# Kernel tuning notes

Measured on AMD Instinct MI355X. Metric: run time of the kernel, lower is better.

## Reference

```python
import jax, jax.numpy as jnp
import numpy as np

B, S, L = 256, 2048, 64  # batch, seq_len, label_size (= num_labels + 2)
START, END = L - 2, L - 1


def setup_inputs() -> dict:
    key = jax.random.key(0)
    k1, k2, k3, k4 = jax.random.split(key, 4)
    logits = jax.random.normal(k1, (B, S, L), dtype=jnp.float32)
    # pad_logits: <SOS>/<EOS> score columns are -100
    logits = logits.at[:, :, START:].set(-100.0)
    transition = jax.random.normal(k2, (L, L), dtype=jnp.float32)
    # CRF.initialize(): nothing transitions into end-as-source / out of start-as-target
    transition = transition.at[:, END].set(-100.0)
    transition = transition.at[START, :].set(-100.0)
    labels = jax.random.randint(k3, (B, S), 0, L - 2, dtype=jnp.int32)
    lens = jnp.maximum(jax.random.randint(k4, (B,), 1, S + 1, dtype=jnp.int32), 1)
    return {"logits": logits, "transition": transition, "labels": labels, "lens": lens}


def _loglik(logits, transition, labels, lens):
    Bc, Sc, Lc = logits.shape
    dt = logits.dtype
    mask_s = (jnp.arange(Sc)[None, :] < lens[:, None])  # [B,S] valid-token mask

    # ---- gold unary score: sum_t logits[b, t, labels[b,t]] over valid t ----
    unary = jnp.take_along_axis(logits, labels[..., None].astype(jnp.int32), axis=2)[..., 0]
    gold_unary = jnp.sum(unary * mask_s.astype(dt), axis=1)  # [B]

    # ---- gold binary score: transition[to, from] along extended label path ----
    lab_ext = jnp.concatenate(
        [jnp.full((Bc, 1), START, labels.dtype), labels, jnp.full((Bc, 1), END, labels.dtype)],
        axis=1,
    )  # [B, S+2]
    m_ext = jnp.arange(Sc + 2)[None, :] < (lens + 1)[:, None]
    lab_ext = jnp.where(m_ext, lab_ext, END)  # positions past lens become <EOS>
    trn_scr = transition[lab_ext[:, 1:], lab_ext[:, :-1]]  # [B, S+1]
    m_trn = (jnp.arange(Sc + 1)[None, :] < (lens + 1)[:, None]).astype(dt)
    gold_binary = jnp.sum(trn_scr * m_trn, axis=1)  # [B]
    gold = gold_unary + gold_binary

    # ---- norm score: forward algorithm (log-semiring scan over time) ----
    alpha0 = jnp.full((Bc, Lc), -100.0, dtype=dt).at[:, START].set(0.0)

    def step(alpha, inp):
        logit, active = inp  # logit: [B,L], active: [B]
        # mat[b, to, frm] = logit[b,to] + alpha[b,frm] + transition[to,frm]
        mat = logit[:, :, None] + alpha[:, None, :] + transition[None, :, :]
        alpha_nxt = jax.nn.logsumexp(mat, axis=2)  # [B,L]
        alpha = jnp.where(active[:, None], alpha_nxt, alpha)
        return alpha, None

    alpha, _ = jax.lax.scan(step, alpha0, (jnp.swapaxes(logits, 0, 1), mask_s.T))
    norm = jax.nn.logsumexp(alpha + transition[END][None, :], axis=1)  # [B]

    return gold - norm


def reference(logits, transition, labels, lens):
    return _loglik(logits, transition, labels, lens)
```

## Files before the change

kernel.cpp:

```cpp
#include <hip/hip_runtime.h>


#define Bsz 256
#define Ssz 2048
#define START_ 62
#define END_ 63
#define PSTRIDE 36

typedef __attribute__((ext_vector_type(2))) _Float16 half2v;
typedef __attribute__((ext_vector_type(8))) _Float16 half8;
typedef __attribute__((ext_vector_type(16))) float f32x16;

__device__ __forceinline__ unsigned pack_pkrtz(float a, float b) {
    auto h = __builtin_amdgcn_cvt_pkrtz(a, b);
    return __builtin_bit_cast(unsigned, h);
}

__device__ __forceinline__ float dot2h(unsigned a, unsigned b, float c) {
#if __has_builtin(__builtin_amdgcn_fdot2)
    return __builtin_amdgcn_fdot2(__builtin_bit_cast(half2v, a),
                                  __builtin_bit_cast(half2v, b), c, false);
#else
    half2v ha = __builtin_bit_cast(half2v, a);
    half2v hb = __builtin_bit_cast(half2v, b);
    c = __builtin_fmaf((float)ha.x, (float)hb.x, c);
    return __builtin_fmaf((float)ha.y, (float)hb.y, c);
#endif
}

__device__ __forceinline__ float wave_sum(float v) {
#pragma unroll
    for (int m = 32; m >= 1; m >>= 1) v += __shfl_xor(v, m, 64);
    return v;
}

#define CRF_STEP(LG)                                                           \
    {                                                                          \
        const float l_ = __builtin_amdgcn_exp2f((LG) * L2E);                   \
        const int nbi_ = __builtin_amdgcn_update_dpp(                          \
            0, __float_as_int(E), 0xB1, 0xf, 0xf, true);                       \
        const unsigned packed_ = pack_pkrtz(E, __int_as_float(nbi_));          \
        float c0 = 0.f, c1 = 0.f, c2 = 0.f, c3 = 0.f;                          \
        float c4 = 0.f, c5 = 0.f, c6 = 0.f, c7 = 0.f;                          \
        _Pragma("unroll")                                                      \
        for (int k8 = 0; k8 < 8; ++k8) {                                       \
            const uint4 q_ = q[k8];                                            \
            const unsigned t0 = (unsigned)__builtin_amdgcn_readlane(           \
                (int)packed_, 8 * k8 + 0);                                     \
            const unsigned t1 = (unsigned)__builtin_amdgcn_readlane(           \
                (int)packed_, 8 * k8 + 2);                                     \
            const unsigned t2 = (unsigned)__builtin_amdgcn_readlane(           \
                (int)packed_, 8 * k8 + 4);                                     \
            const unsigned t3 = (unsigned)__builtin_amdgcn_readlane(           \
                (int)packed_, 8 * k8 + 6);                                     \
            if (k8 & 1) {                                                      \
                c4 = dot2h(t0, q_.x, c4);                                      \
                c5 = dot2h(t1, q_.y, c5);                                      \
                c6 = dot2h(t2, q_.z, c6);                                      \
                c7 = dot2h(t3, q_.w, c7);                                      \
            } else {                                                           \
                c0 = dot2h(t0, q_.x, c0);                                      \
                c1 = dot2h(t1, q_.y, c1);                                      \
                c2 = dot2h(t2, q_.z, c2);                                      \
                c3 = dot2h(t3, q_.w, c3);                                      \
            }                                                                  \
        }                                                                      \
        const float y_ = ((c0 + c1) + (c2 + c3)) + ((c4 + c5) + (c6 + c7));    \
        const float Ey_ = y_ * l_;                                             \
        const int pb_ = __builtin_amdgcn_readlane(__float_as_int(Ey_), 0);     \
        const int ee_ = (pb_ >> 23) & 0xff;                                    \
        const float sc_ = __int_as_float((244 - ee_) << 23);                   \
        E = Ey_ * sc_;                                                         \
        D += ee_ - 117;                                                        \
    }

#define LOAD_QBLOCK()                                                          \
    {                                                                          \
        unsigned off_ = (unsigned)(lane * (PSTRIDE * 4));                      \
        asm volatile("" : "+v"(off_));                                         \
        const uint4* prow_ = (const uint4*)((const char*)Psh + off_);          \
        _Pragma("unroll")                                                      \
        for (int k8 = 0; k8 < 8; ++k8) q[k8] = prow_[k8];                      \
    }

__global__ __launch_bounds__(64)
__attribute__((amdgpu_waves_per_eu(1, 1)))
void crf_kernel(const float* __restrict__ logits,
                const float* __restrict__ transition,
                const int* __restrict__ labels,
                const int* __restrict__ lens,
                float* __restrict__ out)
{
    const int b    = blockIdx.x;
    const int lane = threadIdx.x;
    const float L2E = 1.4426950408889634f;
    const float LN2 = 0.6931471805599453f;

    __shared__ unsigned Psh[64 * PSTRIDE];

    const int len = lens[b];
    const float* lrow = logits + (size_t)b * (Ssz * 64);

#pragma unroll
    for (int k = 0; k < 32; ++k) {
        float p0 = __builtin_amdgcn_exp2f(transition[lane * 64 + 2 * k]     * L2E);
        float p1 = __builtin_amdgcn_exp2f(transition[lane * 64 + 2 * k + 1] * L2E);
        Psh[lane * PSTRIDE + k] = pack_pkrtz(p0, p1);
    }
    asm volatile("s_waitcnt lgkmcnt(0)" ::: "memory");

    float E = (lane == START_) ? 1.0f : 0.0f;
    int   D = 0;

    float lgb[8];
#pragma unroll
    for (int d = 0; d < 8; ++d) {
        int s0 = (d < len) ? d : (len - 1);
        lgb[d] = lrow[s0 * 64 + lane];
    }

    uint4 q[8];
    const int len8 = len & ~7;
    for (int s = 0; s < len8; s += 8) {
        LOAD_QBLOCK();
#pragma unroll
        for (int d = 0; d < 8; ++d) {
            const float lg = lgb[d];
            int pf = s + 8 + d;
            pf = (pf < len) ? pf : (len - 1);
            lgb[d] = lrow[pf * 64 + lane];
            CRF_STEP(lg);
        }
    }
    const int rem = len - len8;
    if (rem) {
        LOAD_QBLOCK();
        for (int d = 0; d < rem; ++d) {
            const float lg = lgb[d];
            CRF_STEP(lg);
        }
    }

    const float Pend = __builtin_amdgcn_exp2f(transition[END_ * 64 + lane] * L2E);
    const float tot  = wave_sum(E * Pend);
    const float norm = LN2 * ((float)D + __builtin_amdgcn_logf(tot));

    const int* lab = labels + (size_t)b * Ssz;
    float g = 0.0f;
    for (int s = lane; s < len; s += 64) {
        const int l1 = lab[s];
        const int l0 = (s == 0) ? START_ : lab[s - 1];
        g += lrow[s * 64 + l1] + transition[l1 * 64 + l0];
    }
    if (lane == 0) g += transition[END_ * 64 + lab[len - 1]];
    const float gold = wave_sum(g);

    if (lane == 0) out[b] = gold - norm;
}


#define MF16(Aop, Bop, Cop) \
    __builtin_amdgcn_mfma_f32_32x32x16_f16((Aop), (Bop), (Cop), 0, 0, 0)

#define STEP_COMPUTE(LGA, LGB)                                                 \
    f32x16 a00, a10;                                                           \
    {                                                                          \
        const float ncf_ = -(float)ci;                                         \
        const float lv0_ = __builtin_amdgcn_exp2f(                             \
            __builtin_fmaf((LGA), L2E, ncf_));                                 \
        const float lv1_ = __builtin_amdgcn_exp2f(                             \
            __builtin_fmaf((LGB), L2E, ncf_));                                 \
        D += ci;                                                               \
        const _Float16 h0_ = (_Float16)lv0_;                                   \
        const _Float16 h1_ = (_Float16)lv1_;                                   \
        const half8 sv0_ = {h0_, h0_, h0_, h0_, h0_, h0_, h0_, h0_};           \
        const half8 sv1_ = {h1_, h1_, h1_, h1_, h1_, h1_, h1_, h1_};           \
        half8 A_;                                                              \
        __builtin_amdgcn_s_setprio(1);                                         \
        A_ = __builtin_bit_cast(half8, PF[0][0]) * sv0_;                       \
        a00 = MF16(A_, __builtin_bit_cast(half8, Bf[0]), Z);                   \
        A_ = __builtin_bit_cast(half8, PF[0][1]) * sv0_;                       \
        a00 = MF16(A_, __builtin_bit_cast(half8, Bf[1]), a00);                 \
        A_ = __builtin_bit_cast(half8, PF[0][2]) * sv0_;                       \
        a00 = MF16(A_, __builtin_bit_cast(half8, Bf[2]), a00);                 \
        A_ = __builtin_bit_cast(half8, PF[0][3]) * sv0_;                       \
        a00 = MF16(A_, __builtin_bit_cast(half8, Bf[3]), a00);                 \
        A_ = __builtin_bit_cast(half8, PF[1][0]) * sv1_;                       \
        a10 = MF16(A_, __builtin_bit_cast(half8, Bf[0]), Z);                   \
        A_ = __builtin_bit_cast(half8, PF[1][1]) * sv1_;                       \
        a10 = MF16(A_, __builtin_bit_cast(half8, Bf[1]), a10);                 \
        A_ = __builtin_bit_cast(half8, PF[1][2]) * sv1_;                       \
        a10 = MF16(A_, __builtin_bit_cast(half8, Bf[2]), a10);                 \
        A_ = __builtin_bit_cast(half8, PF[1][3]) * sv1_;                       \
        a10 = MF16(A_, __builtin_bit_cast(half8, Bf[3]), a10);                 \
        __builtin_amdgcn_s_setprio(0);                                         \
        const float t0_ = fmaxf(fmaxf(a00[0], a00[1]), a00[2]);                \
        const float t1_ = fmaxf(fmaxf(a00[3], a00[4]), a00[5]);                \
        const float t2_ = fmaxf(fmaxf(a00[6], a00[7]), a00[8]);                \
        const float t3_ = fmaxf(fmaxf(a00[9], a00[10]), a00[11]);              \
        const float t4_ = fmaxf(fmaxf(a00[12], a00[13]), a00[14]);             \
        const float ma_ = fmaxf(fmaxf(t0_, t1_), t2_);                         \
        const float mb2_ = fmaxf(fmaxf(t3_, t4_), a00[15]);                    \
        const int mb_ = __builtin_amdgcn_readfirstlane(                        \
            __float_as_int(fmaxf(ma_, mb2_)));                                 \
        int cin_ = ((mb_ >> 23) & 0xff) - 121;      \
        cin_ = (cin_ < -60) ? -60 : cin_;                                      \
        ci = (cin_ > 60) ? 60 : cin_;                                          \
    }

#define TILE_TO_FRAGS(ACC, BD0, BD1)                                           \
    {                                                                          \
        (BD0) = make_uint4(pack_pkrtz(ACC[0], ACC[1]),                         \
                           pack_pkrtz(ACC[2], ACC[3]),                         \
                           pack_pkrtz(ACC[4], ACC[5]),                         \
                           pack_pkrtz(ACC[6], ACC[7]));                        \
        (BD1) = make_uint4(pack_pkrtz(ACC[8], ACC[9]),                         \
                           pack_pkrtz(ACC[10], ACC[11]),                       \
                           pack_pkrtz(ACC[12], ACC[13]),                       \
                           pack_pkrtz(ACC[14], ACC[15]));                      \
    }

#define STEP_FULL(LGA, LGB)                                                    \
    {                                                                          \
        STEP_COMPUTE(LGA, LGB);                                                \
        TILE_TO_FRAGS(a00, Bf[0], Bf[1]);                                      \
        TILE_TO_FRAGS(a10, Bf[2], Bf[3]);                                      \
    }

#define STEP_LAST(LGA, LGB)                                                    \
    {                                                                          \
        STEP_COMPUTE(LGA, LGB);                                                \
        float* gout_ = Gws + (size_t)gslot * 4096 + nb * 32;                   \
        _Pragma("unroll")                                                      \
        for (int r = 0; r < 16; ++r) {                                         \
            const int row0_ = (r & 3) + 8 * (r >> 2) + 4 * hi;                 \
            gout_[row0_ * 64 + lo5]        = a00[r];                           \
            gout_[(row0_ + 32) * 64 + lo5] = a10[r];                           \
        }                                                                      \
        if (lo5 == 0 && hi == 0) Dws[gslot * 2 + nb] = D;                      \
    }

template<int CHT>
__global__ __launch_bounds__(128)
__attribute__((amdgpu_waves_per_eu(4, 8)))
void crf_chunk(const float* __restrict__ logits,
               const float* __restrict__ transition,
               const int* __restrict__ lens,
               float* __restrict__ Gws,
               int* __restrict__ Dws)
{
    const int NCc  = Ssz / CHT;
    const int idx  = blockIdx.x;
    const int c    = idx >> 8;
    const int b    = ((idx & 255) + 37 * c) & 255;
    const int nb   = threadIdx.x >> 6;
    const int lane = threadIdx.x & 63;
    const int lo5  = lane & 31;
    const int hi   = lane >> 5;
    const float L2E = 1.4426950408889634f;

    const int len   = lens[b];
    const int s0    = c * CHT;
    const int gslot = b * NCc + c;
    if (s0 >= len) {
        if (lane == 0) Dws[gslot * 2 + nb] = 0;
        return;
    }
    const int s1 = (s0 + CHT < len) ? (s0 + CHT) : len;

    uint4 PF[2][4];
#pragma unroll
    for (int m = 0; m < 2; ++m) {
#pragma unroll
        for (int kb = 0; kb < 4; ++kb) {
            const float* tp = transition + (m * 32 + lo5) * 64 + kb * 16 + 4 * hi;
            const float e0 = __builtin_amdgcn_exp2f(tp[0] * L2E);
            const float e1 = __builtin_amdgcn_exp2f(tp[1] * L2E);
            const float e2 = __builtin_amdgcn_exp2f(tp[2] * L2E);
            const float e3 = __builtin_amdgcn_exp2f(tp[3] * L2E);
            const float e4 = __builtin_amdgcn_exp2f(tp[8] * L2E);
            const float e5 = __builtin_amdgcn_exp2f(tp[9] * L2E);
            const float e6 = __builtin_amdgcn_exp2f(tp[10] * L2E);
            const float e7 = __builtin_amdgcn_exp2f(tp[11] * L2E);
            PF[m][kb] = make_uint4(pack_pkrtz(e0, e1), pack_pkrtz(e2, e3),
                                   pack_pkrtz(e4, e5), pack_pkrtz(e6, e7));
        }
    }

    uint4 Bf[4];
#pragma unroll
    for (int kb = 0; kb < 4; ++kb) {
        const int col = nb * 32 + lo5;
        unsigned dw[4];
#pragma unroll
        for (int j = 0; j < 4; ++j) {
            const int k0 = kb * 16 + 4 * hi + (j >> 1) * 8 + (j & 1) * 2;
            const unsigned lo16 = (k0     == col) ? 0x3C00u : 0u;
            const unsigned hi16 = (k0 + 1 == col) ? 0x3C00u : 0u;
            dw[j] = lo16 | (hi16 << 16);
        }
        Bf[kb] = make_uint4(dw[0], dw[1], dw[2], dw[3]);
    }

    float z0 = 0.0f;
    asm volatile("" : "+v"(z0));
    f32x16 Z;
#pragma unroll
    for (int i = 0; i < 16; ++i) Z[i] = z0;

    int D  = 0;
    int ci = 0;

    const float* lrow = logits + (size_t)b * (Ssz * 64);
#define CLMP(x) (((x) < s1) ? (x) : (s1 - 1))

    float pA0, pA1, pA2, pA3, pB0, pB1, pB2, pB3;
    {
        int sI;
        sI = CLMP(s0 + 0); pA0 = lrow[sI * 64 + lo5]; pB0 = lrow[sI * 64 + 32 + lo5];
        sI = CLMP(s0 + 1); pA1 = lrow[sI * 64 + lo5]; pB1 = lrow[sI * 64 + 32 + lo5];
        sI = CLMP(s0 + 2); pA2 = lrow[sI * 64 + lo5]; pB2 = lrow[sI * 64 + 32 + lo5];
        sI = CLMP(s0 + 3); pA3 = lrow[sI * 64 + lo5]; pB3 = lrow[sI * 64 + 32 + lo5];
    }

    const int nfull = (s1 - s0) - 1;
    int t = 0;
    for (; t + 4 <= nfull; t += 4) {
        const int sp = s0 + t + 4;
        const int q0i = CLMP(sp), q1i = CLMP(sp + 1), q2i = CLMP(sp + 2), q3i = CLMP(sp + 3);
        const float nA0 = lrow[q0i * 64 + lo5], nB0 = lrow[q0i * 64 + 32 + lo5];
        const float nA1 = lrow[q1i * 64 + lo5], nB1 = lrow[q1i * 64 + 32 + lo5];
        const float nA2 = lrow[q2i * 64 + lo5], nB2 = lrow[q2i * 64 + 32 + lo5];
        const float nA3 = lrow[q3i * 64 + lo5], nB3 = lrow[q3i * 64 + 32 + lo5];
        STEP_FULL(pA0, pB0);
        STEP_FULL(pA1, pB1);
        STEP_FULL(pA2, pB2);
        STEP_FULL(pA3, pB3);
        pA0 = nA0; pB0 = nB0; pA1 = nA1; pB1 = nB1;
        pA2 = nA2; pB2 = nB2; pA3 = nA3; pB3 = nB3;
    }
    const int r_ = nfull - t;
    if (r_ >= 1) STEP_FULL(pA0, pB0);
    if (r_ >= 2) STEP_FULL(pA1, pB1);
    if (r_ >= 3) STEP_FULL(pA2, pB2);

    float fA = pA0, fB = pB0;
    if (r_ == 1) { fA = pA1; fB = pB1; }
    else if (r_ == 2) { fA = pA2; fB = pB2; }
    else if (r_ == 3) { fA = pA3; fB = pB3; }
    STEP_LAST(fA, fB);
#undef CLMP
}

template<int CHT>
__global__ __launch_bounds__(128)
__attribute__((amdgpu_waves_per_eu(1, 2)))
void crf_combine(const float* __restrict__ logits,
                 const float* __restrict__ transition,
                 const int* __restrict__ labels,
                 const int* __restrict__ lens,
                 const float* __restrict__ Gws,
                 const int* __restrict__ Dws,
                 float* __restrict__ out)
{
    const int NCc  = Ssz / CHT;
    const int b    = blockIdx.x;
    const int wid  = threadIdx.x >> 6;
    const int lane = threadIdx.x & 63;
    const float L2E = 1.4426950408889634f;
    const float LN2 = 0.6931471805599453f;
    const int len = lens[b];
    const float* lrow = logits + (size_t)b * (Ssz * 64);

    __shared__ float s_gold;
    float norm = 0.0f;

    if (wid == 1) {
        const int* lab = labels + (size_t)b * Ssz;
        float g = 0.0f;
#pragma unroll 4
        for (int s = lane; s < len; s += 64) {
            const int l1 = lab[s];
            const int l0 = (s == 0) ? START_ : lab[s - 1];
            g += lrow[s * 64 + l1] + transition[l1 * 64 + l0];
        }
        if (lane == 0) g += transition[END_ * 64 + lab[len - 1]];
        const float gold = wave_sum(g);
        if (lane == 0) s_gold = gold;
    } else {
        float E = (lane == START_) ? 1.0f : 0.0f;
        int Dtot = 0;
#pragma unroll 1
        for (int c = 0; c < NCc; ++c) {
            if (c * CHT >= len) break;
            const float4* g4 =
                (const float4*)(Gws + (size_t)(b * NCc + c) * 4096 + lane * 64);
            float4 gr[16];
#pragma unroll
            for (int jj = 0; jj < 16; ++jj) gr[jj] = g4[jj];

            const int Ei = __float_as_int(E);
            float Ens[4] = {0.f, 0.f, 0.f, 0.f};
#pragma unroll
            for (int gq = 0; gq < 4; ++gq) {
#pragma unroll
                for (int qq = 0; qq < 4; ++qq) {
                    const int jj = 4 * gq + qq;
                    Ens[gq] = __builtin_fmaf(gr[jj].x,
                        __int_as_float(__builtin_amdgcn_readlane(Ei, 4 * jj + 0)), Ens[gq]);
                    Ens[gq] = __builtin_fmaf(gr[jj].y,
                        __int_as_float(__builtin_amdgcn_readlane(Ei, 4 * jj + 1)), Ens[gq]);
                    Ens[gq] = __builtin_fmaf(gr[jj].z,
                        __int_as_float(__builtin_amdgcn_readlane(Ei, 4 * jj + 2)), Ens[gq]);
                    Ens[gq] = __builtin_fmaf(gr[jj].w,
                        __int_as_float(__builtin_amdgcn_readlane(Ei, 4 * jj + 3)), Ens[gq]);
                }
            }
            const int D0 = Dws[(b * NCc + c) * 2 + 0];
            const int D1 = Dws[(b * NCc + c) * 2 + 1];
            const int Dm = (D0 > D1) ? D0 : D1;
            const int e0 = 127 + D0 - Dm, e1 = 127 + D1 - Dm;
            const float sc0 = (e0 > 0) ? __int_as_float(e0 << 23) : 0.0f;
            const float sc1 = (e1 > 0) ? __int_as_float(e1 << 23) : 0.0f;
            const float En = (Ens[0] + Ens[1]) * sc0 + (Ens[2] + Ens[3]) * sc1;
            Dtot += Dm;

            float mxv = En;
#pragma unroll
            for (int m = 32; m >= 1; m >>= 1) mxv = fmaxf(mxv, __shfl_xor(mxv, m, 64));
            const int ee = (__float_as_int(mxv) >> 23) & 0xff;
            const float scn = __int_as_float((254 - ee) << 23);
            E = En * scn;
            Dtot += ee - 127;
        }

        const float Pend = __builtin_amdgcn_exp2f(transition[END_ * 64 + lane] * L2E);
        const float tot  = wave_sum(E * Pend);
        norm = LN2 * ((float)Dtot + __builtin_amdgcn_logf(tot));
    }

    __syncthreads();
    if (wid == 0 && lane == 0) out[b] = s_gold - norm;
}

extern "C" void kernel_launch(void* const* d_in, const int* in_sizes, int n_in,
                              void* d_out, int out_size, void* d_ws, size_t ws_size,
                              hipStream_t stream) {
    const float* logits     = (const float*)d_in[0];
    const float* transition = (const float*)d_in[1];
    const int*   labels     = (const int*)d_in[2];
    const int*   lens       = (const int*)d_in[3];
    float*       out        = (float*)d_out;

    const size_t g16  = (size_t)Bsz * 16 * 4096 * sizeof(float);
    const size_t n16  = g16 + (size_t)Bsz * 16 * 2 * sizeof(int);
    const size_t g8   = (size_t)Bsz * 8 * 4096 * sizeof(float);
    const size_t n8   = g8 + (size_t)Bsz * 8 * 2 * sizeof(int);

    if (d_ws != nullptr && ws_size >= n16) {
        float* Gws = (float*)d_ws;
        int*   Dws = (int*)((char*)d_ws + g16);
        crf_chunk<128><<<dim3(Bsz * 16), dim3(128), 0, stream>>>(
            logits, transition, lens, Gws, Dws);
        crf_combine<128><<<dim3(Bsz), dim3(128), 0, stream>>>(
            logits, transition, labels, lens, Gws, Dws, out);
    } else if (d_ws != nullptr && ws_size >= n8) {
        float* Gws = (float*)d_ws;
        int*   Dws = (int*)((char*)d_ws + g8);
        crf_chunk<256><<<dim3(Bsz * 8), dim3(128), 0, stream>>>(
            logits, transition, lens, Gws, Dws);
        crf_combine<256><<<dim3(Bsz), dim3(128), 0, stream>>>(
            logits, transition, labels, lens, Gws, Dws, out);
    } else {
        crf_kernel<<<dim3(Bsz), dim3(64), 0, stream>>>(
            logits, transition, labels, lens, out);
    }
}
```

Before: 320.6 us.

## Switch chunk scan to 16x16x32 MFMA with per-column rescaling

The chunk kernel's transfer-matrix product now uses 16x16x32 f16 MFMAs instead of 32x32x16, and each 64-thread workgroup handles one 32-column half as its own block. The old single per-step scale exponent is replaced by a separate exponent for each 16-column group, and the combine kernel now reads 64 per-column exponents and reconciles them with a wave max. The goal is shorter MFMA dependency chains and more independent waves in flight during the sequential scan. The cost is more exp and scale work per step, cross-lane shuffles for the max, clamping of the exponent input at 14, and a larger exponent workspace.

```diff
diff --git a/kernel.cpp b/kernel.cpp
--- a/kernel.cpp
+++ b/kernel.cpp
@@ -9,7 +9,7 @@
 
 typedef __attribute__((ext_vector_type(2))) _Float16 half2v;
 typedef __attribute__((ext_vector_type(8))) _Float16 half8;
-typedef __attribute__((ext_vector_type(16))) float f32x16;
+typedef __attribute__((ext_vector_type(4))) float f32x4;
 
 __device__ __forceinline__ unsigned pack_pkrtz(float a, float b) {
     auto h = __builtin_amdgcn_cvt_pkrtz(a, b);
@@ -159,89 +159,101 @@
 }
 
 
-#define MF16(Aop, Bop, Cop) \
-    __builtin_amdgcn_mfma_f32_32x32x16_f16((Aop), (Bop), (Cop), 0, 0, 0)
-
-#define STEP_COMPUTE(LGA, LGB)                                                 \
-    f32x16 a00, a10;                                                           \
+#define MF1616(Aop, Bop, Cop) \
+    __builtin_amdgcn_mfma_f32_16x16x32_f16((Aop), (Bop), (Cop), 0, 0, 0)
+
+#define CRF2_COMPUTE(LGP)                                                      \
+    f32x4 acc[4][2];                                                           \
+    float scv[2];                                                              \
     {                                                                          \
-        const float ncf_ = -(float)ci;                                         \
-        const float lv0_ = __builtin_amdgcn_exp2f(                             \
-            __builtin_fmaf((LGA), L2E, ncf_));                                 \
-        const float lv1_ = __builtin_amdgcn_exp2f(                             \
-            __builtin_fmaf((LGB), L2E, ncf_));                                 \
-        D += ci;                                                               \
-        const _Float16 h0_ = (_Float16)lv0_;                                   \
-        const _Float16 h1_ = (_Float16)lv1_;                                   \
-        const half8 sv0_ = {h0_, h0_, h0_, h0_, h0_, h0_, h0_, h0_};           \
-        const half8 sv1_ = {h1_, h1_, h1_, h1_, h1_, h1_, h1_, h1_};           \
-        half8 A_;                                                              \
-        __builtin_amdgcn_s_setprio(1);                                         \
-        A_ = __builtin_bit_cast(half8, PF[0][0]) * sv0_;                       \
-        a00 = MF16(A_, __builtin_bit_cast(half8, Bf[0]), Z);                   \
-        A_ = __builtin_bit_cast(half8, PF[0][1]) * sv0_;                       \
-        a00 = MF16(A_, __builtin_bit_cast(half8, Bf[1]), a00);                 \
-        A_ = __builtin_bit_cast(half8, PF[0][2]) * sv0_;                       \
-        a00 = MF16(A_, __builtin_bit_cast(half8, Bf[2]), a00);                 \
-        A_ = __builtin_bit_cast(half8, PF[0][3]) * sv0_;                       \
-        a00 = MF16(A_, __builtin_bit_cast(half8, Bf[3]), a00);                 \
-        A_ = __builtin_bit_cast(half8, PF[1][0]) * sv1_;                       \
-        a10 = MF16(A_, __builtin_bit_cast(half8, Bf[0]), Z);                   \
-        A_ = __builtin_bit_cast(half8, PF[1][1]) * sv1_;                       \
-        a10 = MF16(A_, __builtin_bit_cast(half8, Bf[1]), a10);                 \
-        A_ = __builtin_bit_cast(half8, PF[1][2]) * sv1_;                       \
-        a10 = MF16(A_, __builtin_bit_cast(half8, Bf[2]), a10);                 \
-        A_ = __builtin_bit_cast(half8, PF[1][3]) * sv1_;                       \
-        a10 = MF16(A_, __builtin_bit_cast(half8, Bf[3]), a10);                 \
-        __builtin_amdgcn_s_setprio(0);                                         \
-        const float t0_ = fmaxf(fmaxf(a00[0], a00[1]), a00[2]);                \
-        const float t1_ = fmaxf(fmaxf(a00[3], a00[4]), a00[5]);                \
-        const float t2_ = fmaxf(fmaxf(a00[6], a00[7]), a00[8]);                \
-        const float t3_ = fmaxf(fmaxf(a00[9], a00[10]), a00[11]);              \
-        const float t4_ = fmaxf(fmaxf(a00[12], a00[13]), a00[14]);             \
-        const float ma_ = fmaxf(fmaxf(t0_, t1_), t2_);                         \
-        const float mb2_ = fmaxf(fmaxf(t3_, t4_), a00[15]);                    \
-        const int mb_ = __builtin_amdgcn_readfirstlane(                        \
-            __float_as_int(fmaxf(ma_, mb2_)));                                 \
-        int cin_ = ((mb_ >> 23) & 0xff) - 121;      \
-        cin_ = (cin_ < -60) ? -60 : cin_;                                      \
-        ci = (cin_ > 60) ? 60 : cin_;                                          \
-    }
-
-#define TILE_TO_FRAGS(ACC, BD0, BD1)                                           \
+        unsigned hh_[4];                                                       \
+        _Pragma("unroll")                                                      \
+        for (int rt = 0; rt < 4; ++rt) {                                       \
+            const float lv_ = __builtin_amdgcn_exp2f(                          \
+                fminf((LGP)[rt] * L2E, 14.0f));                                \
+            hh_[rt] = pack_pkrtz(lv_, lv_);                                    \
+        }                                                                      \
+        _Pragma("unroll")                                                      \
+        for (int rt = 0; rt < 4; ++rt) {                                       \
+            const half2v hp_ = __builtin_bit_cast(half2v, hh_[rt]);            \
+            const half8 hs_ = {hp_.x, hp_.x, hp_.x, hp_.x,                     \
+                               hp_.x, hp_.x, hp_.x, hp_.x};                    \
+            const half8 A0_ = __builtin_bit_cast(half8, PF[rt][0]) * hs_;      \
+            const half8 A1_ = __builtin_bit_cast(half8, PF[rt][1]) * hs_;      \
+            _Pragma("unroll")                                                  \
+            for (int ct = 0; ct < 2; ++ct) {                                   \
+                const uint4 b1_ = make_uint4(Bf[1][ct][0], Bf[1][ct][1],       \
+                                             Bf[1][ct][2], Bf[1][ct][3]);      \
+                const uint4 b0_ = make_uint4(Bf[0][ct][0], Bf[0][ct][1],       \
+                                             Bf[0][ct][2], Bf[0][ct][3]);      \
+                f32x4 t_ = MF1616(A1_, __builtin_bit_cast(half8, b1_), Z4);    \
+                acc[rt][ct] =                                                  \
+                    MF1616(A0_, __builtin_bit_cast(half8, b0_), t_);           \
+            }                                                                  \
+        }                                                                      \
+        _Pragma("unroll")                                                      \
+        for (int ct = 0; ct < 2; ++ct) {                                       \
+            const float u0_ = fmaxf(fmaxf(acc[0][ct][0], acc[0][ct][1]),       \
+                                    acc[0][ct][2]);                            \
+            const float u1_ = fmaxf(fmaxf(acc[0][ct][3], acc[1][ct][0]),       \
+                                    acc[1][ct][1]);                            \
+            const float u2_ = fmaxf(fmaxf(acc[1][ct][2], acc[1][ct][3]),       \
+                                    acc[2][ct][0]);                            \
+            const float u3_ = fmaxf(fmaxf(acc[2][ct][1], acc[2][ct][2]),       \
+                                    acc[2][ct][3]);                            \
+            const float u4_ = fmaxf(fmaxf(acc[3][ct][0], acc[3][ct][1]),       \
+                                    acc[3][ct][2]);                            \
+            float m_ = fmaxf(fmaxf(fmaxf(u0_, u1_), u2_),                      \
+                             fmaxf(fmaxf(u3_, u4_), acc[3][ct][3]));           \
+            m_ = fmaxf(m_, __shfl_xor(m_, 16, 64));                            \
+            m_ = fmaxf(m_, __shfl_xor(m_, 32, 64));                            \
+            const int ee_ = (__float_as_int(m_) >> 23) & 0xff;                 \
+            scv[ct] = __int_as_float((248 - ee_) << 23);       \
+            if (ct == 0) D0 += ee_ - 121; else D1 += ee_ - 121;                \
+        }                                                                      \
+    }
+
+#define CRF2_STEP(LGP)                                                         \
     {                                                                          \
-        (BD0) = make_uint4(pack_pkrtz(ACC[0], ACC[1]),                         \
-                           pack_pkrtz(ACC[2], ACC[3]),                         \
-                           pack_pkrtz(ACC[4], ACC[5]),                         \
-                           pack_pkrtz(ACC[6], ACC[7]));                        \
-        (BD1) = make_uint4(pack_pkrtz(ACC[8], ACC[9]),                         \
-                           pack_pkrtz(ACC[10], ACC[11]),                       \
-                           pack_pkrtz(ACC[12], ACC[13]),                       \
-                           pack_pkrtz(ACC[14], ACC[15]));                      \
-    }
-
-#define STEP_FULL(LGA, LGB)                                                    \
+        CRF2_COMPUTE(LGP);                                                     \
+        _Pragma("unroll")                                                      \
+        for (int ct = 0; ct < 2; ++ct) {                                       \
+            const float s_ = scv[ct];                                          \
+            _Pragma("unroll")                                                  \
+            for (int rt = 0; rt < 4; ++rt) {                                   \
+                Bf[rt >> 1][ct][(rt & 1) * 2 + 0] =                            \
+                    pack_pkrtz(acc[rt][ct][0] * s_, acc[rt][ct][1] * s_);      \
+                Bf[rt >> 1][ct][(rt & 1) * 2 + 1] =                            \
+                    pack_pkrtz(acc[rt][ct][2] * s_, acc[rt][ct][3] * s_);      \
+            }                                                                  \
+        }                                                                      \
+    }
+
+#define CRF2_LAST(LGP)                                                         \
     {                                                                          \
-        STEP_COMPUTE(LGA, LGB);                                                \
-        TILE_TO_FRAGS(a00, Bf[0], Bf[1]);                                      \
-        TILE_TO_FRAGS(a10, Bf[2], Bf[3]);                                      \
-    }
-
-#define STEP_LAST(LGA, LGB)                                                    \
-    {                                                                          \
-        STEP_COMPUTE(LGA, LGB);                                                \
-        float* gout_ = Gws + (size_t)gslot * 4096 + nb * 32;                   \
-        _Pragma("unroll")                                                      \
-        for (int r = 0; r < 16; ++r) {                                         \
-            const int row0_ = (r & 3) + 8 * (r >> 2) + 4 * hi;                 \
-            gout_[row0_ * 64 + lo5]        = a00[r];                           \
-            gout_[(row0_ + 32) * 64 + lo5] = a10[r];                           \
-        }                                                                      \
-        if (lo5 == 0 && hi == 0) Dws[gslot * 2 + nb] = D;                      \
+        CRF2_COMPUTE(LGP);                                                     \
+        float* gout_ = Gws + (size_t)gslot * 4096;                             \
+        _Pragma("unroll")                                                      \
+        for (int ct = 0; ct < 2; ++ct) {                                       \
+            const float s_ = scv[ct];                                          \
+            const int col_ = nb * 32 + ct * 16 + lo4;                          \
+            _Pragma("unroll")                                                  \
+            for (int rt = 0; rt < 4; ++rt) {                                   \
+                _Pragma("unroll")                                              \
+                for (int j = 0; j < 4; ++j) {                                  \
+                    gout_[(16 * rt + 4 * gq + j) * 64 + col_] =                \
+                        acc[rt][ct][j] * s_;                                   \
+                }                                                              \
+            }                                                                  \
+        }                                                                      \
+        if (gq == 0) {                                                         \
+            Dws[(size_t)gslot * 64 + nb * 32 + lo4]      = D0;                 \
+            Dws[(size_t)gslot * 64 + nb * 32 + 16 + lo4] = D1;                 \
+        }                                                                      \
     }
 
 template<int CHT>
-__global__ __launch_bounds__(128)
+__global__ __launch_bounds__(64)
 __attribute__((amdgpu_waves_per_eu(4, 8)))
 void crf_chunk(const float* __restrict__ logits,
                const float* __restrict__ transition,
@@ -251,104 +263,100 @@
 {
     const int NCc  = Ssz / CHT;
     const int idx  = blockIdx.x;
-    const int c    = idx >> 8;
-    const int b    = ((idx & 255) + 37 * c) & 255;
-    const int nb   = threadIdx.x >> 6;
-    const int lane = threadIdx.x & 63;
-    const int lo5  = lane & 31;
-    const int hi   = lane >> 5;
+    const int nb   = idx & 1;
+    const int tq   = idx >> 1;
+    const int c    = tq >> 8;
+    const int b    = ((tq & 255) + 37 * c) & 255;
+    const int lane = threadIdx.x;
+    const int lo4  = lane & 15;
+    const int gq   = lane >> 4;
     const float L2E = 1.4426950408889634f;
 
     const int len   = lens[b];
     const int s0    = c * CHT;
     const int gslot = b * NCc + c;
-    if (s0 >= len) {
-        if (lane == 0) Dws[gslot * 2 + nb] = 0;
-        return;
-    }
+    if (s0 >= len) return;
     const int s1 = (s0 + CHT < len) ? (s0 + CHT) : len;
 
-    uint4 PF[2][4];
-#pragma unroll
-    for (int m = 0; m < 2; ++m) {
-#pragma unroll
-        for (int kb = 0; kb < 4; ++kb) {
-            const float* tp = transition + (m * 32 + lo5) * 64 + kb * 16 + 4 * hi;
-            const float e0 = __builtin_amdgcn_exp2f(tp[0] * L2E);
-            const float e1 = __builtin_amdgcn_exp2f(tp[1] * L2E);
-            const float e2 = __builtin_amdgcn_exp2f(tp[2] * L2E);
-            const float e3 = __builtin_amdgcn_exp2f(tp[3] * L2E);
-            const float e4 = __builtin_amdgcn_exp2f(tp[8] * L2E);
-            const float e5 = __builtin_amdgcn_exp2f(tp[9] * L2E);
-            const float e6 = __builtin_amdgcn_exp2f(tp[10] * L2E);
-            const float e7 = __builtin_amdgcn_exp2f(tp[11] * L2E);
-            PF[m][kb] = make_uint4(pack_pkrtz(e0, e1), pack_pkrtz(e2, e3),
-                                   pack_pkrtz(e4, e5), pack_pkrtz(e6, e7));
-        }
-    }
-
-    uint4 Bf[4];
-#pragma unroll
-    for (int kb = 0; kb < 4; ++kb) {
-        const int col = nb * 32 + lo5;
-        unsigned dw[4];
-#pragma unroll
-        for (int j = 0; j < 4; ++j) {
-            const int k0 = kb * 16 + 4 * hi + (j >> 1) * 8 + (j & 1) * 2;
-            const unsigned lo16 = (k0     == col) ? 0x3C00u : 0u;
-            const unsigned hi16 = (k0 + 1 == col) ? 0x3C00u : 0u;
-            dw[j] = lo16 | (hi16 << 16);
-        }
-        Bf[kb] = make_uint4(dw[0], dw[1], dw[2], dw[3]);
+    uint4 PF[4][2];
+#pragma unroll
+    for (int rt = 0; rt < 4; ++rt) {
+#pragma unroll
+        for (int kb = 0; kb < 2; ++kb) {
+            const float* tp =
+                transition + (16 * rt + lo4) * 64 + 32 * kb + 4 * gq;
+            unsigned dw[4];
+            const int off_[4] = {0, 2, 16, 18};
+#pragma unroll
+            for (int d = 0; d < 4; ++d) {
+                const float e0 = __builtin_amdgcn_exp2f(
+                    fminf(tp[off_[d]] * L2E, 14.0f));
+                const float e1 = __builtin_amdgcn_exp2f(
+                    fminf(tp[off_[d] + 1] * L2E, 14.0f));
+                dw[d] = pack_pkrtz(e0, e1);
+            }
+            PF[rt][kb] = make_uint4(dw[0], dw[1], dw[2], dw[3]);
+        }
+    }
+
+    unsigned Bf[2][2][4];
+#pragma unroll
+    for (int kb = 0; kb < 2; ++kb) {
+#pragma unroll
+        for (int ct = 0; ct < 2; ++ct) {
+            const int col = nb * 32 + ct * 16 + lo4;
+#pragma unroll
+            for (int d = 0; d < 4; ++d) {
+                const int f0 = 2 * d, f1 = 2 * d + 1;
+                const int k0 = 32 * kb + 4 * gq + (f0 & 3) + 16 * (f0 >> 2);
+                const int k1 = 32 * kb + 4 * gq + (f1 & 3) + 16 * (f1 >> 2);
+                const unsigned lo16 = (k0 == col) ? 0x3C00u : 0u;
+                const unsigned hi16 = (k1 == col) ? 0x3C00u : 0u;
+                Bf[kb][ct][d] = lo16 | (hi16 << 16);
+            }
+        }
     }
 
     float z0 = 0.0f;
     asm volatile("" : "+v"(z0));
-    f32x16 Z;
-#pragma unroll
-    for (int i = 0; i < 16; ++i) Z[i] = z0;
-
-    int D  = 0;
-    int ci = 0;
+    const f32x4 Z4 = {z0, z0, z0, z0};
+
+    int D0 = 0, D1 = 0;
 
     const float* lrow = logits + (size_t)b * (Ssz * 64);
 #define CLMP(x) (((x) < s1) ? (x) : (s1 - 1))
 
-    float pA0, pA1, pA2, pA3, pB0, pB1, pB2, pB3;
+    float lgA[4], lgB[4];
     {
-        int sI;
-        sI = CLMP(s0 + 0); pA0 = lrow[sI * 64 + lo5]; pB0 = lrow[sI * 64 + 32 + lo5];
-        sI = CLMP(s0 + 1); pA1 = lrow[sI * 64 + lo5]; pB1 = lrow[sI * 64 + 32 + lo5];
-        sI = CLMP(s0 + 2); pA2 = lrow[sI * 64 + lo5]; pB2 = lrow[sI * 64 + 32 + lo5];
-        sI = CLMP(s0 + 3); pA3 = lrow[sI * 64 + lo5]; pB3 = lrow[sI * 64 + 32 + lo5];
+        const int sa = CLMP(s0), sb = CLMP(s0 + 1);
+#pragma unroll
+        for (int rt = 0; rt < 4; ++rt) {
+            lgA[rt] = lrow[sa * 64 + 16 * rt + lo4];
+            lgB[rt] = lrow[sb * 64 + 16 * rt + lo4];
+        }
     }
 
     const int nfull = (s1 - s0) - 1;
     int t = 0;
-    for (; t + 4 <= nfull; t += 4) {
-        const int sp = s0 + t + 4;
-        const int q0i = CLMP(sp), q1i = CLMP(sp + 1), q2i = CLMP(sp + 2), q3i = CLMP(sp + 3);
-        const float nA0 = lrow[q0i * 64 + lo5], nB0 = lrow[q0i * 64 + 32 + lo5];
-        const float nA1 = lrow[q1i * 64 + lo5], nB1 = lrow[q1i * 64 + 32 + lo5];
-        const float nA2 = lrow[q2i * 64 + lo5], nB2 = lrow[q2i * 64 + 32 + lo5];
-        const float nA3 = lrow[q3i * 64 + lo5], nB3 = lrow[q3i * 64 + 32 + lo5];
-        STEP_FULL(pA0, pB0);
-        STEP_FULL(pA1, pB1);
-        STEP_FULL(pA2, pB2);
-        STEP_FULL(pA3, pB3);
-        pA0 = nA0; pB0 = nB0; pA1 = nA1; pB1 = nB1;
-        pA2 = nA2; pB2 = nB2; pA3 = nA3; pB3 = nB3;
-    }
-    const int r_ = nfull - t;
-    if (r_ >= 1) STEP_FULL(pA0, pB0);
-    if (r_ >= 2) STEP_FULL(pA1, pB1);
-    if (r_ >= 3) STEP_FULL(pA2, pB2);
-
-    float fA = pA0, fB = pB0;
-    if (r_ == 1) { fA = pA1; fB = pB1; }
-    else if (r_ == 2) { fA = pA2; fB = pB2; }
-    else if (r_ == 3) { fA = pA3; fB = pB3; }
-    STEP_LAST(fA, fB);
+    for (; t + 2 <= nfull; t += 2) {
+        const int q0 = CLMP(s0 + t + 2), q1 = CLMP(s0 + t + 3);
+        float nA[4], nB[4];
+#pragma unroll
+        for (int rt = 0; rt < 4; ++rt) {
+            nA[rt] = lrow[q0 * 64 + 16 * rt + lo4];
+            nB[rt] = lrow[q1 * 64 + 16 * rt + lo4];
+        }
+        CRF2_STEP(lgA);
+        CRF2_STEP(lgB);
+#pragma unroll
+        for (int rt = 0; rt < 4; ++rt) { lgA[rt] = nA[rt]; lgB[rt] = nB[rt]; }
+    }
+    if (nfull - t >= 1) {
+        CRF2_STEP(lgA);
+        CRF2_LAST(lgB);
+    } else {
+        CRF2_LAST(lgA);
+    }
 #undef CLMP
 }
 
@@ -399,7 +407,18 @@
 #pragma unroll
             for (int jj = 0; jj < 16; ++jj) gr[jj] = g4[jj];
 
-            const int Ei = __float_as_int(E);
+            const int Dc = Dws[(size_t)(b * NCc + c) * 64 + lane];
+            int Dm = Dc;
+#pragma unroll
+            for (int m = 32; m >= 1; m >>= 1) {
+                const int o = __shfl_xor(Dm, m, 64);
+                Dm = (o > Dm) ? o : Dm;
+            }
+            int es = 127 + Dc - Dm;
+            es = (es < 0) ? 0 : es;
+            const float Ef = E * __int_as_float(es << 23);
+
+            const int Ei = __float_as_int(Ef);
             float Ens[4] = {0.f, 0.f, 0.f, 0.f};
 #pragma unroll
             for (int gq = 0; gq < 4; ++gq) {
@@ -416,13 +435,7 @@
                         __int_as_float(__builtin_amdgcn_readlane(Ei, 4 * jj + 3)), Ens[gq]);
                 }
             }
-            const int D0 = Dws[(b * NCc + c) * 2 + 0];
-            const int D1 = Dws[(b * NCc + c) * 2 + 1];
-            const int Dm = (D0 > D1) ? D0 : D1;
-            const int e0 = 127 + D0 - Dm, e1 = 127 + D1 - Dm;
-            const float sc0 = (e0 > 0) ? __int_as_float(e0 << 23) : 0.0f;
-            const float sc1 = (e1 > 0) ? __int_as_float(e1 << 23) : 0.0f;
-            const float En = (Ens[0] + Ens[1]) * sc0 + (Ens[2] + Ens[3]) * sc1;
+            const float En = (Ens[0] + Ens[1]) + (Ens[2] + Ens[3]);
             Dtot += Dm;
 
             float mxv = En;
@@ -453,21 +466,21 @@
     float*       out        = (float*)d_out;
 
     const size_t g16  = (size_t)Bsz * 16 * 4096 * sizeof(float);
-    const size_t n16  = g16 + (size_t)Bsz * 16 * 2 * sizeof(int);
+    const size_t n16  = g16 + (size_t)Bsz * 16 * 64 * sizeof(int);
     const size_t g8   = (size_t)Bsz * 8 * 4096 * sizeof(float);
-    const size_t n8   = g8 + (size_t)Bsz * 8 * 2 * sizeof(int);
+    const size_t n8   = g8 + (size_t)Bsz * 8 * 64 * sizeof(int);
 
     if (d_ws != nullptr && ws_size >= n16) {
         float* Gws = (float*)d_ws;
         int*   Dws = (int*)((char*)d_ws + g16);
-        crf_chunk<128><<<dim3(Bsz * 16), dim3(128), 0, stream>>>(
+        crf_chunk<128><<<dim3(Bsz * 16 * 2), dim3(64), 0, stream>>>(
             logits, transition, lens, Gws, Dws);
         crf_combine<128><<<dim3(Bsz), dim3(128), 0, stream>>>(
             logits, transition, labels, lens, Gws, Dws, out);
     } else if (d_ws != nullptr && ws_size >= n8) {
         float* Gws = (float*)d_ws;
         int*   Dws = (int*)((char*)d_ws + g8);
-        crf_chunk<256><<<dim3(Bsz * 8), dim3(128), 0, stream>>>(
+        crf_chunk<256><<<dim3(Bsz * 8 * 2), dim3(64), 0, stream>>>(
             logits, transition, lens, Gws, Dws);
         crf_combine<256><<<dim3(Bsz), dim3(128), 0, stream>>>(
             logits, transition, labels, lens, Gws, Dws, out);
```

After: 400.3 us. +24.9%, slower.
